# Kernel tuning notes

Hardware: AMD Instinct MI355X
Metric: run time of the kernel (lower is better)

## Reference

```python
import jax, jax.numpy as jnp
import numpy as np

B, M, N, DQ, H = 4, 4096, 4096, 256, 64

def setup_inputs() -> dict:
    key = jax.random.key(0)
    k1, k2, k3, k4 = jax.random.split(key, 4)
    x = jax.random.normal(k1, (B, M, DQ), dtype=jnp.float32)
    cond = jax.random.normal(k2, (B, N, DQ), dtype=jnp.float32)
    Wq = jax.random.normal(k3, (DQ, H), dtype=jnp.float32) * (1.0 / np.sqrt(DQ))
    Wkv = jax.random.normal(k4, (DQ, 2 * H), dtype=jnp.float32) * (1.0 / np.sqrt(DQ))
    return {"x": x, "cond": cond, "Wq": Wq, "Wkv": Wkv}

def reference(x, cond, Wq, Wkv):
    h = Wq.shape[1]
    q = jnp.einsum('bmi,ih->bmh', x, Wq)          # [B,M,H]
    kv = jnp.einsum('bni,ih->bnh', cond, Wkv)     # [B,N,2H]
    k, v = jnp.split(kv, 2, axis=-1)              # each [B,N,H]
    qk = jnp.einsum('bmd,bnd->bmn', q, k) / jnp.sqrt(jnp.asarray(h, q.dtype))
    attn = jax.nn.softmax(qk, axis=-1)            # [B,M,N]
    out = jnp.einsum('bmn,bnd->bmd', attn, v)     # [B,M,H]
    return out
```

## Files before the change

kernel.cpp:

```cpp
#include <hip/hip_runtime.h>
#include <hip/hip_bf16.h>
#include <cstdint>


#define BB 4
#define MM 4096
#define NN 4096
#define DQm 256
#define DH 64
#define NSP 8
#define KVT (64 / NSP)
#define QSCALE 0.18033688011112042f

typedef _Float16 half8 __attribute__((ext_vector_type(8)));
typedef _Float16 half4 __attribute__((ext_vector_type(4)));
typedef float floatx16 __attribute__((ext_vector_type(16)));

static __device__ __forceinline__ unsigned pkrtz(float a, float b) {
    union { __fp16 h __attribute__((ext_vector_type(2))); unsigned u; } cv;
    cv.h = __builtin_amdgcn_cvt_pkrtz(a, b);
    return cv.u;
}

__global__ __launch_bounds__(256) void wtrans_kernel(const float* __restrict__ Wq,
                                                     const float* __restrict__ Wkv,
                                                     _Float16* __restrict__ wt) {
    int cout = blockIdx.x;
    int t = threadIdx.x;
    float v = (cout < 64) ? Wq[t * 64 + cout] * QSCALE : Wkv[t * 128 + (cout - 64)];
    _Float16 hi = (_Float16)v;
    _Float16 lo = (_Float16)(v - (float)hi);
    wt[cout * DQm + t] = hi;
    wt[192 * DQm + cout * DQm + t] = lo;
}

__global__ __launch_bounds__(256, 3) void proj_kernel(const float* __restrict__ x,
                                                      const float* __restrict__ cond,
                                                      const _Float16* __restrict__ wt,
                                                      _Float16* __restrict__ q_h,
                                                      _Float16* __restrict__ k_h,
                                                      _Float16* __restrict__ vt_h) {
    const int t = threadIdx.x;
    const int w = t >> 6, lane = t & 63, c = lane & 31, h = lane >> 5;
    const int W = blockIdx.x * 4 + w;
    const bool isq = W < 1024;
    int rowtile, colbase;
    const float* src;
    if (isq) { rowtile = W >> 1; colbase = (W & 1) * 32; src = x; }
    else { int W2 = W - 1024; rowtile = W2 >> 2; colbase = (W2 & 3) * 32; src = cond; }
    const long rowbase = (long)rowtile * 32;
    const float* arow = src + (rowbase + c) * DQm;
    const _Float16* bh_p = wt + (long)((isq ? 0 : 64) + colbase + c) * DQm;
    const _Float16* bl_p = bh_p + 192 * DQm;

    floatx16 a1, a2, a3;
#pragma unroll
    for (int i = 0; i < 16; ++i) { a1[i] = 0.f; a2[i] = 0.f; a3[i] = 0.f; }
#pragma unroll
    for (int kt = 0; kt < 16; ++kt) {
        const int off = kt * 16 + h * 8;
        float4 v0 = *(const float4*)(arow + off);
        float4 v1 = *(const float4*)(arow + off + 4);
        half8 ah = {(_Float16)v0.x, (_Float16)v0.y, (_Float16)v0.z, (_Float16)v0.w,
                    (_Float16)v1.x, (_Float16)v1.y, (_Float16)v1.z, (_Float16)v1.w};
        half8 al = {(_Float16)(v0.x - (float)ah[0]), (_Float16)(v0.y - (float)ah[1]),
                    (_Float16)(v0.z - (float)ah[2]), (_Float16)(v0.w - (float)ah[3]),
                    (_Float16)(v1.x - (float)ah[4]), (_Float16)(v1.y - (float)ah[5]),
                    (_Float16)(v1.z - (float)ah[6]), (_Float16)(v1.w - (float)ah[7])};
        half8 bh = *(const half8*)(bh_p + off);
        half8 bl = *(const half8*)(bl_p + off);
        a1 = __builtin_amdgcn_mfma_f32_32x32x16_f16(ah, bh, a1, 0, 0, 0);
        a2 = __builtin_amdgcn_mfma_f32_32x32x16_f16(ah, bl, a2, 0, 0, 0);
        a3 = __builtin_amdgcn_mfma_f32_32x32x16_f16(al, bh, a3, 0, 0, 0);
    }

    if (isq) {
#pragma unroll
        for (int r = 0; r < 16; ++r) {
            int m = (r & 3) + 8 * (r >> 2) + 4 * h;
            q_h[(rowbase + m) * DH + colbase + c] =
                (_Float16)(a1[r] + a2[r] + a3[r]);
        }
    } else {
        int cout = colbase + c;
        if (cout < 64) {
#pragma unroll
            for (int r = 0; r < 16; ++r) {
                int m = (r & 3) + 8 * (r >> 2) + 4 * h;
                k_h[(rowbase + m) * DH + cout] =
                    (_Float16)(a1[r] + a2[r] + a3[r]);
            }
        } else {
            int d = cout - 64;
            long bb = rowbase >> 12;
#pragma unroll
            for (int s2 = 0; s2 < 4; ++s2) {
                long n = rowbase + 8 * s2 + 4 * h;
                half4 hv;
#pragma unroll
                for (int j = 0; j < 4; ++j)
                    hv[j] = (_Float16)(a1[s2 * 4 + j] + a2[s2 * 4 + j] + a3[s2 * 4 + j]);
                *(half4*)(vt_h + (bb * DH + d) * NN + (n & 4095)) = hv;
            }
        }
    }
}

__global__ __launch_bounds__(256, 4) void fa_kernel(const _Float16* __restrict__ q_h,
                                                    const _Float16* __restrict__ k_h,
                                                    const _Float16* __restrict__ vt_h,
                                                    float* __restrict__ Opart,
                                                    float2* __restrict__ ml) {
    __shared__ __align__(16) _Float16 k_lds[64][72];
    __shared__ __align__(16) _Float16 vt_lds[64][72];

    const int t = threadIdx.x;
    const int w = t >> 6;
    const int lane = t & 63;
    const int c = lane & 31;
    const int h = lane >> 5;

    const int bid = blockIdx.x;
    const int sp = bid >> 7;
    const int b  = (bid >> 5) & 3;
    const int mt = bid & 31;
    const int mbase = mt * 128 + w * 32;
    const long qrow = (long)b * MM + mbase + c;

    half8 qf[4];
#pragma unroll
    for (int kt = 0; kt < 4; ++kt)
        qf[kt] = *(const half8*)(q_h + qrow * DH + kt * 16 + h * 8);

    const uint4* kp = (const uint4*)(k_h + ((long)b * NN + sp * KVT * 64) * DH) + t;
    const _Float16* vbase =
        vt_h + ((long)b * DH + (t >> 3)) * NN + sp * KVT * 64 + (t & 7) * 8;
    const uint4* vp0 = (const uint4*)vbase;
    const uint4* vp1 = (const uint4*)(vbase + 32 * NN);

    uint4 kr0 = kp[0], kr1 = kp[256];
    uint4 vr0 = *vp0, vr1 = *vp1;

    floatx16 Oc0, Oc1;
#pragma unroll
    for (int i = 0; i < 16; ++i) { Oc0[i] = 0.f; Oc1[i] = 0.f; }
    float m_run = -INFINITY, l_run = 0.f;

#pragma unroll 1
    for (int it = 0; it < KVT; ++it) {
        __syncthreads();
        *(uint4*)(&k_lds[t >> 3][(t & 7) * 8]) = kr0;
        *(uint4*)(&k_lds[32 + (t >> 3)][(t & 7) * 8]) = kr1;
        *(uint4*)(&vt_lds[t >> 3][(t & 7) * 8]) = vr0;
        *(uint4*)(&vt_lds[32 + (t >> 3)][(t & 7) * 8]) = vr1;
        kp += 512; vp0 += 8; vp1 += 8;
        if (it < KVT - 1) {
            kr0 = kp[0]; kr1 = kp[256];
            vr0 = *vp0;  vr1 = *vp1;
        }
        __syncthreads();

        floatx16 Sc[2];
#pragma unroll
        for (int a = 0; a < 2; ++a) {
            floatx16 acc;
#pragma unroll
            for (int i = 0; i < 16; ++i) acc[i] = 0.f;
#pragma unroll
            for (int kt = 0; kt < 4; ++kt) {
                half8 af = *(const half8*)(&k_lds[a * 32 + c][kt * 16 + h * 8]);
                acc = __builtin_amdgcn_mfma_f32_32x32x16_f16(af, qf[kt], acc, 0, 0, 0);
            }
            Sc[a] = acc;
        }

        float tmax = -INFINITY;
#pragma unroll
        for (int a = 0; a < 2; ++a)
#pragma unroll
            for (int r = 0; r < 16; ++r) tmax = fmaxf(tmax, Sc[a][r]);
        tmax = fmaxf(tmax, __shfl_xor(tmax, 32, 64));
        float m_new = fmaxf(m_run, tmax);
        float alpha = exp2f(m_run - m_new);
        float tsum = 0.f;
#pragma unroll
        for (int a = 0; a < 2; ++a)
#pragma unroll
            for (int r = 0; r < 16; ++r) {
                float p = exp2f(Sc[a][r] - m_new);
                Sc[a][r] = p;
                tsum += p;
            }
        tsum += __shfl_xor(tsum, 32, 64);
        l_run = l_run * alpha + tsum;
        m_run = m_new;
#pragma unroll
        for (int i = 0; i < 16; ++i) { Oc0[i] *= alpha; Oc1[i] *= alpha; }

#pragma unroll
        for (int a = 0; a < 2; ++a) {
            uint2 pk0 = {pkrtz(Sc[a][0],  Sc[a][1]),  pkrtz(Sc[a][2],  Sc[a][3])};
            uint2 pk1 = {pkrtz(Sc[a][4],  Sc[a][5]),  pkrtz(Sc[a][6],  Sc[a][7])};
            uint2 pk2 = {pkrtz(Sc[a][8],  Sc[a][9]),  pkrtz(Sc[a][10], Sc[a][11])};
            uint2 pk3 = {pkrtz(Sc[a][12], Sc[a][13]), pkrtz(Sc[a][14], Sc[a][15])};
            uint2 s0, s1, ex0, ex1;
            s0.x = h ? pk0.x : pk1.x;  s0.y = h ? pk0.y : pk1.y;
            s1.x = h ? pk2.x : pk3.x;  s1.y = h ? pk2.y : pk3.y;
            ex0.x = __shfl_xor((int)s0.x, 32, 64);
            ex0.y = __shfl_xor((int)s0.y, 32, 64);
            ex1.x = __shfl_xor((int)s1.x, 32, 64);
            ex1.y = __shfl_xor((int)s1.y, 32, 64);
            union { uint4 u; half8 f; } f0, f1;
            f0.u.x = h ? ex0.x : pk0.x;  f0.u.y = h ? ex0.y : pk0.y;
            f0.u.z = h ? pk1.x : ex0.x;  f0.u.w = h ? pk1.y : ex0.y;
            f1.u.x = h ? ex1.x : pk2.x;  f1.u.y = h ? ex1.y : pk2.y;
            f1.u.z = h ? pk3.x : ex1.x;  f1.u.w = h ? pk3.y : ex1.y;
#pragma unroll
            for (int bq = 0; bq < 2; ++bq) {
                int kt = 2 * a + bq;
                half8 pf = bq ? f1.f : f0.f;
                half8 vf0 = *(const half8*)(&vt_lds[c][kt * 16 + h * 8]);
                half8 vf1 = *(const half8*)(&vt_lds[32 + c][kt * 16 + h * 8]);
                Oc0 = __builtin_amdgcn_mfma_f32_32x32x16_f16(vf0, pf, Oc0, 0, 0, 0);
                Oc1 = __builtin_amdgcn_mfma_f32_32x32x16_f16(vf1, pf, Oc1, 0, 0, 0);
            }
        }
    }

    const long obase = ((long)sp * BB * MM + (long)b * MM + mbase + c) * DH;
#pragma unroll
    for (int dt = 0; dt < 2; ++dt) {
        const floatx16& O = dt ? Oc1 : Oc0;
#pragma unroll
        for (int s2 = 0; s2 < 4; ++s2) {
            float4 v;
            v.x = O[s2 * 4 + 0]; v.y = O[s2 * 4 + 1];
            v.z = O[s2 * 4 + 2]; v.w = O[s2 * 4 + 3];
            *(float4*)(Opart + obase + dt * 32 + s2 * 8 + h * 4) = v;
        }
    }
    if (h == 0)
        ml[((long)sp * BB + b) * MM + mbase + c] = make_float2(m_run, l_run);
}

__global__ __launch_bounds__(256) void merge_kernel(const float* __restrict__ Opart,
                                                    const float2* __restrict__ ml,
                                                    float* __restrict__ out) {
    const long gid = (long)blockIdx.x * 256 + threadIdx.x;
    const long row = gid >> 4;
    float2 p[NSP];
    float mmax = -INFINITY;
#pragma unroll
    for (int i = 0; i < NSP; ++i) {
        p[i] = ml[(long)i * BB * MM + row];
        mmax = fmaxf(mmax, p[i].x);
    }
    float denom = 0.f;
    float4 o = {0.f, 0.f, 0.f, 0.f};
#pragma unroll
    for (int i = 0; i < NSP; ++i) {
        float ai = exp2f(p[i].x - mmax);
        denom += ai * p[i].y;
        float4 v = *(const float4*)(Opart + ((long)i * BB * MM * DH) + gid * 4);
        o.x += ai * v.x; o.y += ai * v.y; o.z += ai * v.z; o.w += ai * v.w;
    }
    float inv = 1.f / denom;
    o.x *= inv; o.y *= inv; o.z *= inv; o.w *= inv;
    *(float4*)(out + gid * 4) = o;
}

extern "C" void kernel_launch(void* const* d_in, const int* in_sizes, int n_in,
                              void* d_out, int out_size, void* d_ws, size_t ws_size,
                              hipStream_t stream) {
    const float* x    = (const float*)d_in[0];
    const float* cond = (const float*)d_in[1];
    const float* Wq   = (const float*)d_in[2];
    const float* Wkv  = (const float*)d_in[3];
    float* out = (float*)d_out;

    char* ws = (char*)d_ws;
    _Float16* wt   = (_Float16*)(ws);
    _Float16* q_h  = (_Float16*)(ws + 196608);
    _Float16* k_h  = (_Float16*)(ws + 196608 + 2097152);
    _Float16* vt_h = (_Float16*)(ws + 196608 + 2 * 2097152);
    float*    Op   = (float*)(ws + 196608 + 3 * 2097152);
    float2*   mlp  = (float2*)(ws + 196608 + 3 * 2097152 + (size_t)NSP * 4194304);

    wtrans_kernel<<<192, 256, 0, stream>>>(Wq, Wkv, wt);
    proj_kernel<<<768, 256, 0, stream>>>(x, cond, wt, q_h, k_h, vt_h);
    fa_kernel<<<NSP * BB * 32, 256, 0, stream>>>(q_h, k_h, vt_h, Op, mlp);
    merge_kernel<<<BB * MM * DH / 1024, 256, 0, stream>>>(Op, mlp, out);
}
```

Baseline: 141.3 us.

## Double-buffer K/V tiles in LDS to drop one barrier per iteration

Gives K and V^T two LDS buffers each. Each iteration now writes the next tile into the other buffer while computing on the current one, so one of the two __syncthreads per KV step goes away. Global loads are issued two tiles ahead. This doubles LDS use per block (about 36 KB), which could cut occupancy below the requested 4 blocks per CU.

```diff
diff --git a/kernel.cpp b/kernel.cpp
--- a/kernel.cpp
+++ b/kernel.cpp
@@ -111,8 +111,8 @@
                                                     const _Float16* __restrict__ vt_h,
                                                     float* __restrict__ Opart,
                                                     float2* __restrict__ ml) {
-    __shared__ __align__(16) _Float16 k_lds[64][72];
-    __shared__ __align__(16) _Float16 vt_lds[64][72];
+    __shared__ __align__(16) _Float16 k_lds[2][64][72];
+    __shared__ __align__(16) _Float16 vt_lds[2][64][72];
 
     const int t = threadIdx.x;
     const int w = t >> 6;
@@ -132,14 +132,23 @@
     for (int kt = 0; kt < 4; ++kt)
         qf[kt] = *(const half8*)(q_h + qrow * DH + kt * 16 + h * 8);
 
+    const int sr = t >> 3, sq8 = (t & 7) * 8;
     const uint4* kp = (const uint4*)(k_h + ((long)b * NN + sp * KVT * 64) * DH) + t;
     const _Float16* vbase =
-        vt_h + ((long)b * DH + (t >> 3)) * NN + sp * KVT * 64 + (t & 7) * 8;
+        vt_h + ((long)b * DH + sr) * NN + sp * KVT * 64 + sq8;
     const uint4* vp0 = (const uint4*)vbase;
     const uint4* vp1 = (const uint4*)(vbase + 32 * NN);
 
     uint4 kr0 = kp[0], kr1 = kp[256];
     uint4 vr0 = *vp0, vr1 = *vp1;
+    *(uint4*)(&k_lds[0][sr][sq8]) = kr0;
+    *(uint4*)(&k_lds[0][32 + sr][sq8]) = kr1;
+    *(uint4*)(&vt_lds[0][sr][sq8]) = vr0;
+    *(uint4*)(&vt_lds[0][32 + sr][sq8]) = vr1;
+    kp += 512; vp0 += 8; vp1 += 8;
+    kr0 = kp[0]; kr1 = kp[256];
+    vr0 = *vp0;  vr1 = *vp1;
+    kp += 512; vp0 += 8; vp1 += 8;
 
     floatx16 Oc0, Oc1;
 #pragma unroll
@@ -149,16 +158,18 @@
 #pragma unroll 1
     for (int it = 0; it < KVT; ++it) {
         __syncthreads();
-        *(uint4*)(&k_lds[t >> 3][(t & 7) * 8]) = kr0;
-        *(uint4*)(&k_lds[32 + (t >> 3)][(t & 7) * 8]) = kr1;
-        *(uint4*)(&vt_lds[t >> 3][(t & 7) * 8]) = vr0;
-        *(uint4*)(&vt_lds[32 + (t >> 3)][(t & 7) * 8]) = vr1;
-        kp += 512; vp0 += 8; vp1 += 8;
+        const int cb = it & 1, nb = cb ^ 1;
         if (it < KVT - 1) {
+            *(uint4*)(&k_lds[nb][sr][sq8]) = kr0;
+            *(uint4*)(&k_lds[nb][32 + sr][sq8]) = kr1;
+            *(uint4*)(&vt_lds[nb][sr][sq8]) = vr0;
+            *(uint4*)(&vt_lds[nb][32 + sr][sq8]) = vr1;
+        }
+        if (it < KVT - 2) {
             kr0 = kp[0]; kr1 = kp[256];
             vr0 = *vp0;  vr1 = *vp1;
-        }
-        __syncthreads();
+            kp += 512; vp0 += 8; vp1 += 8;
+        }
 
         floatx16 Sc[2];
 #pragma unroll
@@ -168,7 +179,7 @@
             for (int i = 0; i < 16; ++i) acc[i] = 0.f;
 #pragma unroll
             for (int kt = 0; kt < 4; ++kt) {
-                half8 af = *(const half8*)(&k_lds[a * 32 + c][kt * 16 + h * 8]);
+                half8 af = *(const half8*)(&k_lds[cb][a * 32 + c][kt * 16 + h * 8]);
                 acc = __builtin_amdgcn_mfma_f32_32x32x16_f16(af, qf[kt], acc, 0, 0, 0);
             }
             Sc[a] = acc;
@@ -219,8 +230,8 @@
             for (int bq = 0; bq < 2; ++bq) {
                 int kt = 2 * a + bq;
                 half8 pf = bq ? f1.f : f0.f;
-                half8 vf0 = *(const half8*)(&vt_lds[c][kt * 16 + h * 8]);
-                half8 vf1 = *(const half8*)(&vt_lds[32 + c][kt * 16 + h * 8]);
+                half8 vf0 = *(const half8*)(&vt_lds[cb][c][kt * 16 + h * 8]);
+                half8 vf1 = *(const half8*)(&vt_lds[cb][32 + c][kt * 16 + h * 8]);
                 Oc0 = __builtin_amdgcn_mfma_f32_32x32x16_f16(vf0, pf, Oc0, 0, 0, 0);
                 Oc1 = __builtin_amdgcn_mfma_f32_32x32x16_f16(vf1, pf, Oc1, 0, 0, 0);
             }
```

Result: no change. 143.0 us (+1.2%).
